# Kernel tuning notes

Measured on AMD Instinct MI355X. Metric: run time of the kernel, lower is better.

Reference implementation:

```python
import jax, jax.numpy as jnp
import numpy as np

B, S, IN, EMB, H = 4, 2048, 256, 512, 8
D = EMB // H
SCALE = 1.0 / np.sqrt(EMB)  # source uses 1/sqrt(embed_size), not head_dim
EPS = 1e-5


def setup_inputs() -> dict:
    key = jax.random.key(0)
    ks = jax.random.split(key, 20)
    def w(k, shape, fan_in):
        return jax.random.normal(k, shape, jnp.float32) * (1.0 / np.sqrt(fan_in))
    inp = {"state_emb": jax.random.normal(ks[0], (B, S, IN), jnp.float32)}
    i = 1
    for p in ("q", "k", "v"):
        inp[f"{p}_W1"] = w(ks[i], (IN, EMB), IN); i += 1
        inp[f"{p}_b1"] = jnp.zeros((EMB,), jnp.float32)
        inp[f"{p}_W2"] = w(ks[i], (EMB, EMB), EMB); i += 1
        inp[f"{p}_b2"] = jnp.zeros((EMB,), jnp.float32)
    inp["f_W1"] = w(ks[i], (EMB, 2 * EMB), EMB); i += 1
    inp["f_b1"] = jnp.zeros((2 * EMB,), jnp.float32)
    inp["f_W2"] = w(ks[i], (2 * EMB, EMB), 2 * EMB); i += 1
    inp["f_b2"] = jnp.zeros((EMB,), jnp.float32)
    inp["ln1_g"] = jnp.ones((EMB,), jnp.float32)
    inp["ln1_b"] = jnp.zeros((EMB,), jnp.float32)
    inp["ln2_g"] = jnp.ones((EMB,), jnp.float32)
    inp["ln2_b"] = jnp.zeros((EMB,), jnp.float32)
    return inp


def _mlp2(x, W1, b1, W2, b2):
    return jax.nn.relu(x @ W1 + b1) @ W2 + b2


def _layernorm(x, g, b):
    mu = jnp.mean(x, axis=-1, keepdims=True)
    var = jnp.mean(jnp.square(x - mu), axis=-1, keepdims=True)
    return (x - mu) * jax.lax.rsqrt(var + EPS) * g + b


def reference(state_emb, q_W1, q_b1, q_W2, q_b2, k_W1, k_b1, k_W2, k_b2,
              v_W1, v_b1, v_W2, v_b2, f_W1, f_b1, f_W2, f_b2,
              ln1_g, ln1_b, ln2_g, ln2_b):
    n, dim = state_emb.shape[0], state_emb.shape[1]
    q = _mlp2(state_emb, q_W1, q_b1, q_W2, q_b2)  # [n, dim, EMB]
    k = _mlp2(state_emb, k_W1, k_b1, k_W2, k_b2)
    v = _mlp2(state_emb, v_W1, v_b1, v_W2, v_b2)
    qh = q.reshape(n, dim, H, D)
    kh = k.reshape(n, dim, H, D)
    vh = v.reshape(n, dim, H, D)
    energy = jnp.einsum('nqhd,nkhd->nhqk', qh, kh)  # [n, H, dim, dim]
    attn = jax.nn.softmax(energy * SCALE, axis=-1)
    ctx = jnp.einsum('nhql,nlhd->nqhd', attn, vh).reshape(n, dim, EMB)
    x = _layernorm(ctx + q, ln1_g, ln1_b)  # residual with queries, per source
    ff = _mlp2(x, f_W1, f_b1, f_W2, f_b2)
    return _layernorm(x + ff, ln2_g, ln2_b)
```

## Files before the change

### kernel.cpp

```cpp
#include <hip/hip_runtime.h>
#include <hip/hip_bf16.h>
#include <math.h>

#define BB   4
#define SS   2048
#define INF_ 256
#define EMB  512
#define NH   8
#define HD   64
#define NT   8192

typedef unsigned short u16;
typedef unsigned int   u32;
typedef __attribute__((ext_vector_type(8))) short bf16x8;
typedef __attribute__((ext_vector_type(8))) unsigned short u16x8;
typedef __attribute__((ext_vector_type(4))) float f32x4;

constexpr float C2  = 0.06375871607f;
constexpr float RB  = 0.005624549f;
constexpr float TB  = 1.00390625f;
constexpr float EPS = 1e-5f;

__device__ __forceinline__ u16 f2bf(float v) {
    __hip_bfloat16 h = __float2bfloat16(v);
    return *(u16*)&h;
}
__device__ __forceinline__ float bf2f(u16 u) {
    __hip_bfloat16 h = *(__hip_bfloat16*)&u;
    return __bfloat162float(h);
}
__device__ __forceinline__ u16 ftrunc_bf(float v) {
    return (u16)(__float_as_uint(v * TB) >> 16);
}
__device__ __forceinline__ f32x4 mfma16(bf16x8 a, bf16x8 b, f32x4 c) {
    return __builtin_amdgcn_mfma_f32_16x16x32_bf16(a, b, c, 0, 0, 0);
}
__device__ __forceinline__ void async16(const void* g, void* l) {
    __builtin_amdgcn_global_load_lds(
        (const __attribute__((address_space(1))) void*)g,
        (__attribute__((address_space(3))) void*)l, 16, 0, 0);
}
__device__ __forceinline__ int derive_flag(const u16* x) {
    const int lane = threadIdx.x & 63;
    const unsigned e = (x[lane * 2] >> 7) & 0xFF;
    float pl = (e == 0 || (e >= 110 && e <= 140)) ? 1.0f : 0.0f;
    #pragma unroll
    for (int o = 1; o < 64; o <<= 1) pl += __shfl_xor(pl, o);
    return pl < 32.0f;
}

__global__ __launch_bounds__(256) void prep(
    const u16* __restrict__ xsrc,
    const void* w0, const void* w1, const void* w2, const void* w3,
    const void* w4, const void* w5, const void* w6, const void* w7,
    const void* p0, const void* p1, const void* p2, const void* p3,
    const void* p4, const void* p5, const void* p6, const void* p7,
    const void* p8, const void* p9, const void* p10, const void* p11,
    u16* __restrict__ xbf, u16* __restrict__ wt1, u16* __restrict__ wt2,
    u16* __restrict__ f1t, u16* __restrict__ f2t, float* __restrict__ small)
{
    const int isf = derive_flag(xsrc);
    const int z = blockIdx.z;
    const int tid = threadIdx.x;

    if (z < 8) {
        int K, M; const void* src; u16* dst;
        switch (z) {
            case 0: K=256;  M=512;  src=w0; dst=wt1;             break;
            case 1: K=256;  M=512;  src=w1; dst=wt1+512*256;     break;
            case 2: K=256;  M=512;  src=w2; dst=wt1+2*512*256;   break;
            case 3: K=512;  M=512;  src=w3; dst=wt2;             break;
            case 4: K=512;  M=512;  src=w4; dst=wt2+512*512;     break;
            case 5: K=512;  M=512;  src=w5; dst=wt2+2*512*512;   break;
            case 6: K=512;  M=1024; src=w6; dst=f1t;             break;
            default:K=1024; M=512;  src=w7; dst=f2t;             break;
        }
        const int m0 = blockIdx.x * 32, k0 = blockIdx.y * 32;
        if (m0 >= M || k0 >= K) return;
        __shared__ u16 t[32][33];
        const int tx = tid & 31, ty = tid >> 5;
        #pragma unroll
        for (int i = 0; i < 4; ++i) {
            const int kk = k0 + ty + i * 8;
            t[ty + i * 8][tx] = isf ? ftrunc_bf(((const float*)src)[(size_t)kk * M + m0 + tx])
                                    : ((const u16*)src)[(size_t)kk * M + m0 + tx];
        }
        __syncthreads();
        #pragma unroll
        for (int i = 0; i < 4; ++i) {
            const int mm = m0 + ty + i * 8;
            dst[(size_t)mm * K + k0 + tx] = t[tx][ty + i * 8];
        }
    } else if (z == 8) {
        const int bid = blockIdx.y * 32 + blockIdx.x;
        const int base = bid * 2048 + tid * 8;
        if (isf) {
            #pragma unroll
            for (int j = 0; j < 8; ++j)
                xbf[base + j] = ftrunc_bf(((const float*)xsrc)[base + j]);
        } else {
            *(u16x8*)&xbf[base] = *(const u16x8*)&xsrc[base];
        }
    } else {
        const int bid = blockIdx.y * 32 + blockIdx.x;
        if (bid >= 28) return;
        const int e = bid * 256 + tid;
        int id, i;
        if (e < 3072)      { id = e >> 9;               i = e & 511;          }
        else if (e < 4096) { id = 6;                    i = e - 3072;         }
        else               { id = 7 + ((e - 4096) >> 9); i = (e - 4096) & 511; }
        const void* src;
        switch (id) {
            case 0: src = p0; break;  case 1: src = p1; break;
            case 2: src = p2; break;  case 3: src = p3; break;
            case 4: src = p4; break;  case 5: src = p5; break;
            case 6: src = p6; break;  case 7: src = p7; break;
            case 8: src = p8; break;  case 9: src = p9; break;
            case 10: src = p10; break; default: src = p11; break;
        }
        small[e] = isf ? ((const float*)src)[i] : bf2f(((const u16*)src)[i]);
    }
}

template <int TR, int TC, bool RELU, bool AWHICH, bool VOUT>
__global__ __launch_bounds__(256) void gemm_bt(
    const u16* __restrict__ Aall, const u16* __restrict__ Wtall,
    const float* __restrict__ ball, u16* __restrict__ out,
    u16* __restrict__ vtb, int N, int K, int M)
{
    constexpr int RT = TR / 32, CT = TC / 32;
    constexpr int AR = TR / 32, BR = TC / 32;
    constexpr int SSTAGE = (TR + TC) * 64;
    constexpr int SELEMS = VOUT ? (SSTAGE > TC * 136 ? SSTAGE : TC * 136) : SSTAGE;
    __shared__ __align__(16) u16 smem[SELEMS];
    u16* sA = smem;
    u16* sB = smem + TR * 64;

    const int mtiles = M / TC;
    const int which = blockIdx.x / mtiles;
    const int colb  = blockIdx.x % mtiles;
    const int row0 = blockIdx.y * TR, col0 = colb * TC;
    const u16* A  = Aall + (AWHICH ? (size_t)which * N * K : 0);
    const u16* Wt = Wtall + (size_t)which * M * K;
    const float* bias = ball + (size_t)which * M;

    const int tid = threadIdx.x;
    const int lane = tid & 63, w = tid >> 6;
    const int wrow = (w & 1) * (TR / 2), wcol = (w >> 1) * (TC / 2);
    const int c = lane & 15, quad = lane >> 4;

    const u16* ap[AR]; const u16* bp[BR];
    #pragma unroll
    for (int i = 0; i < AR; ++i) {
        const int raw = i * 256 + tid, r = raw >> 3, ch = (raw & 7) ^ (r & 7);
        ap[i] = A + (size_t)(row0 + r) * K + ch * 8;
    }
    #pragma unroll
    for (int i = 0; i < BR; ++i) {
        const int raw = i * 256 + tid, r = raw >> 3, ch = (raw & 7) ^ (r & 7);
        bp[i] = Wt + (size_t)(col0 + r) * K + ch * 8;
    }

    f32x4 acc[RT][CT] = {};

    for (int k0 = 0; k0 < K; k0 += 64) {
        __syncthreads();
        #pragma unroll
        for (int i = 0; i < AR; ++i) {
            async16(ap[i], (char*)sA + (i * 256 + tid) * 16);
            ap[i] += 64;
        }
        #pragma unroll
        for (int i = 0; i < BR; ++i) {
            async16(bp[i], (char*)sB + (i * 256 + tid) * 16);
            bp[i] += 64;
        }
        __syncthreads();

        #pragma unroll
        for (int kt = 0; kt < 2; ++kt) {
            bf16x8 af[RT], bfr[CT];
            #pragma unroll
            for (int rt = 0; rt < RT; ++rt) {
                const int r = wrow + rt * 16 + c;
                af[rt] = *(const bf16x8*)&sA[(r * 8 + ((kt * 4 + quad) ^ (r & 7))) * 8];
            }
            #pragma unroll
            for (int ct = 0; ct < CT; ++ct) {
                const int r = wcol + ct * 16 + c;
                bfr[ct] = *(const bf16x8*)&sB[(r * 8 + ((kt * 4 + quad) ^ (r & 7))) * 8];
            }
            #pragma unroll
            for (int rt = 0; rt < RT; ++rt)
                #pragma unroll
                for (int ct = 0; ct < CT; ++ct)
                    acc[rt][ct] = mfma16(af[rt], bfr[ct], acc[rt][ct]);
        }
    }

    if (VOUT && which == 2) {
        __syncthreads();
        #pragma unroll
        for (int rt = 0; rt < RT; ++rt) {
            const int rowb = wrow + rt * 16 + quad * 4;
            #pragma unroll
            for (int ct = 0; ct < CT; ++ct) {
                const int col = wcol + ct * 16 + c;
                const float bb = bias[col0 + col];
                ushort4 pk;
                pk.x = ftrunc_bf(acc[rt][ct][0] + bb);
                pk.y = ftrunc_bf(acc[rt][ct][1] + bb);
                pk.z = ftrunc_bf(acc[rt][ct][2] + bb);
                pk.w = ftrunc_bf(acc[rt][ct][3] + bb);
                *(ushort4*)&smem[col * 136 + rowb] = pk;
            }
        }
        __syncthreads();
        const int dl = tid >> 1, half = tid & 1;
        const int hg = (col0 + dl) >> 6, dd = (col0 + dl) & 63;
        const int bb = row0 >> 11, s0 = row0 & 2047;
        u16* dst = vtb + ((size_t)(bb * NH + hg) * HD + dd) * SS + s0 + half * 64;
        #pragma unroll
        for (int j = 0; j < 8; ++j)
            *(u16x8*)&dst[j * 8] = *(const u16x8*)&smem[dl * 136 + half * 64 + j * 8];
        return;
    }

    const size_t outW = (size_t)which * N * M;
    #pragma unroll
    for (int rt = 0; rt < RT; ++rt) {
        #pragma unroll
        for (int i = 0; i < 4; ++i) {
            const int row = row0 + wrow + rt * 16 + quad * 4 + i;
            #pragma unroll
            for (int ct = 0; ct < CT; ++ct) {
                const int col = col0 + wcol + ct * 16 + c;
                float v = acc[rt][ct][i] + bias[col];
                if (RELU) v = fmaxf(v, 0.0f);
                out[outW + (size_t)row * M + col] = ftrunc_bf(v);
            }
        }
    }
}

__global__ __launch_bounds__(256) void attn_mfma(
    const u16* __restrict__ q, const u16* __restrict__ k,
    const u16* __restrict__ vt, u16* __restrict__ ctx)
{
    __shared__ __align__(16) u16 sK[2][64 * 64];
    __shared__ __align__(16) u16 sV[2][64 * 64];
    __shared__ __align__(16) u16 sP[4][16 * 64];

    const int tid = threadIdx.x;
    const int w = tid >> 6, lane = tid & 63;
    const int c = lane & 15, quad = lane >> 4;
    const int id = blockIdx.x;
    const int slot = id >> 3;
    const int bh = ((id & 7) << 2) | (slot >> 5);
    const int qt = slot & 31;
    const int b = bh >> 3, h = bh & 7;
    const int q0 = qt * 64;
    const size_t tokbase = (size_t)b * SS;
    const int hoff = h * HD;

    const int myq = q0 + w * 16 + c;
    bf16x8 qf[2];
    #pragma unroll
    for (int kt = 0; kt < 2; ++kt)
        qf[kt] = *(const bf16x8*)&q[(tokbase + myq) * EMB + hoff + kt * 32 + quad * 8];

    const u16* kp[2]; const u16* vp[2];
    #pragma unroll
    for (int i = 0; i < 2; ++i) {
        const int raw = i * 256 + tid, rr = raw >> 3, ch = (raw & 7) ^ (rr & 7);
        kp[i] = k + (tokbase + rr) * EMB + hoff + ch * 8;
        vp[i] = vt + ((size_t)(b * NH + h) * HD + rr) * SS + ch * 8;
    }
    auto stage = [&](int buf) {
        #pragma unroll
        for (int i = 0; i < 2; ++i) {
            async16(kp[i], (char*)&sK[buf][0] + (i * 256 + tid) * 16);
            kp[i] += 64 * EMB;
        }
        #pragma unroll
        for (int i = 0; i < 2; ++i) {
            async16(vp[i], (char*)&sV[buf][0] + (i * 256 + tid) * 16);
            vp[i] += 64;
        }
    };
    stage(0);

    float l_lane = 0.0f;
    f32x4 accO[4] = {};

    for (int t = 0; t < SS / 64; ++t) {
        __syncthreads();
        const int buf = t & 1;
        if (t + 1 < SS / 64) stage(buf ^ 1);

        f32x4 accS[4] = {};
        #pragma unroll
        for (int mt = 0; mt < 4; ++mt) {
            const int key = mt * 16 + c;
            #pragma unroll
            for (int kt = 0; kt < 2; ++kt) {
                bf16x8 kf = *(const bf16x8*)&sK[buf][(key * 8 + ((kt * 4 + quad) ^ (key & 7))) * 8];
                accS[mt] = mfma16(kf, qf[kt], accS[mt]);
            }
        }

        u32 pw[8];
        float ls = 0.0f;
        #pragma unroll
        for (int mt = 0; mt < 4; ++mt) {
            const float e0 = __builtin_amdgcn_exp2f(fmaf(accS[mt][0], C2, RB));
            const float e1 = __builtin_amdgcn_exp2f(fmaf(accS[mt][1], C2, RB));
            const float e2 = __builtin_amdgcn_exp2f(fmaf(accS[mt][2], C2, RB));
            const float e3 = __builtin_amdgcn_exp2f(fmaf(accS[mt][3], C2, RB));
            ls += (e0 + e1) + (e2 + e3);
            pw[2 * mt]     = __builtin_amdgcn_perm(__float_as_uint(e1), __float_as_uint(e0), 0x07060302u);
            pw[2 * mt + 1] = __builtin_amdgcn_perm(__float_as_uint(e3), __float_as_uint(e2), 0x07060302u);
        }
        l_lane += ls;

        #pragma unroll
        for (int mt = 0; mt < 4; ++mt) {
            const int chunkW = 2 * mt + (quad >> 1);
            const int blk = c * 8 + (chunkW ^ (c & 7));
            uint2 u; u.x = pw[2 * mt]; u.y = pw[2 * mt + 1];
            *(uint2*)((char*)&sP[w][0] + blk * 16 + 8 * (quad & 1)) = u;
        }

        bf16x8 pf[2];
        #pragma unroll
        for (int kt = 0; kt < 2; ++kt)
            pf[kt] = *(const bf16x8*)&sP[w][(c * 8 + ((kt * 4 + quad) ^ (c & 7))) * 8];
        #pragma unroll
        for (int nt = 0; nt < 4; ++nt) {
            const int d = nt * 16 + c;
            #pragma unroll
            for (int kt = 0; kt < 2; ++kt) {
                bf16x8 vf = *(const bf16x8*)&sV[buf][(d * 8 + ((kt * 4 + quad) ^ (d & 7))) * 8];
                accO[nt] = mfma16(vf, pf[kt], accO[nt]);
            }
        }
    }

    float l = l_lane;
    l += __shfl_xor(l, 16);
    l += __shfl_xor(l, 32);
    const float li = (l > 0.0f) ? (1.0f / l) : 0.0f;

    const int tok = q0 + w * 16 + c;
    u16* dst = ctx + (tokbase + tok) * EMB + hoff + quad * 4;
    #pragma unroll
    for (int nt = 0; nt < 4; ++nt) {
        ushort4 pk;
        pk.x = ftrunc_bf(accO[nt][0] * li);
        pk.y = ftrunc_bf(accO[nt][1] * li);
        pk.z = ftrunc_bf(accO[nt][2] * li);
        pk.w = ftrunc_bf(accO[nt][3] * li);
        *(ushort4*)&dst[nt * 16] = pk;
    }
}

__global__ __launch_bounds__(256) void ln_mid(
    const u16* __restrict__ a, const u16* __restrict__ b2,
    const float* __restrict__ g, const float* __restrict__ be,
    u16* __restrict__ outb)
{
    const int wave = threadIdx.x >> 6, lane = threadIdx.x & 63;
    const size_t row = (size_t)blockIdx.x * 4 + wave;
    const u16x8 av = *(const u16x8*)&a[row * EMB + lane * 8];
    const u16x8 bv = *(const u16x8*)&b2[row * EMB + lane * 8];
    float vals[8], sum = 0.0f;
    #pragma unroll
    for (int i = 0; i < 8; ++i) { vals[i] = bf2f(av[i]) + bf2f(bv[i]); sum += vals[i]; }
    #pragma unroll
    for (int o = 1; o < 64; o <<= 1) sum += __shfl_xor(sum, o);
    const float mu = sum * (1.0f / 512.0f);
    float vs = 0.0f;
    #pragma unroll
    for (int i = 0; i < 8; ++i) { const float d = vals[i] - mu; vs += d * d; }
    #pragma unroll
    for (int o = 1; o < 64; o <<= 1) vs += __shfl_xor(vs, o);
    const float rstd = rsqrtf(vs * (1.0f / 512.0f) + EPS);
    u16x8 ov;
    #pragma unroll
    for (int i = 0; i < 8; ++i) {
        const int col = lane * 8 + i;
        ov[i] = f2bf((vals[i] - mu) * rstd * g[col] + be[col]);
    }
    *(u16x8*)&outb[row * EMB + lane * 8] = ov;
}

__global__ __launch_bounds__(256) void ln_final(
    const u16* __restrict__ a, const u16* __restrict__ b2,
    const float* __restrict__ g, const float* __restrict__ be,
    void* __restrict__ dout, const u16* __restrict__ xsrc)
{
    const int isf = derive_flag(xsrc);
    const int wave = threadIdx.x >> 6, lane = threadIdx.x & 63;
    const size_t row = (size_t)blockIdx.x * 4 + wave;
    const u16x8 av = *(const u16x8*)&a[row * EMB + lane * 8];
    const u16x8 bv = *(const u16x8*)&b2[row * EMB + lane * 8];
    float vals[8], sum = 0.0f;
    #pragma unroll
    for (int i = 0; i < 8; ++i) { vals[i] = bf2f(av[i]) + bf2f(bv[i]); sum += vals[i]; }
    #pragma unroll
    for (int o = 1; o < 64; o <<= 1) sum += __shfl_xor(sum, o);
    const float mu = sum * (1.0f / 512.0f);
    float vs = 0.0f;
    #pragma unroll
    for (int i = 0; i < 8; ++i) { const float d = vals[i] - mu; vs += d * d; }
    #pragma unroll
    for (int o = 1; o < 64; o <<= 1) vs += __shfl_xor(vs, o);
    const float rstd = rsqrtf(vs * (1.0f / 512.0f) + EPS);
    if (isf) {
        #pragma unroll
        for (int i = 0; i < 8; ++i) {
            const int col = lane * 8 + i;
            ((float*)dout)[row * EMB + col] = (vals[i] - mu) * rstd * g[col] + be[col];
        }
    } else {
        u16x8 ov;
        #pragma unroll
        for (int i = 0; i < 8; ++i) {
            const int col = lane * 8 + i;
            ov[i] = f2bf((vals[i] - mu) * rstd * g[col] + be[col]);
        }
        *(u16x8*)&((u16*)dout)[row * EMB + lane * 8] = ov;
    }
}

extern "C" void kernel_launch(void* const* d_in, const int* in_sizes, int n_in,
                              void* d_out, int out_size, void* d_ws, size_t ws_size,
                              hipStream_t stream)
{
    char* ws = (char*)d_ws;
    float* small = (float*)(ws + 0);
    u16*   wt1   = (u16*)(ws + 32768);
    u16*   wt2   = (u16*)(ws + 819200);
    u16*   f1t   = (u16*)(ws + 2392064);
    u16*   f2t   = (u16*)(ws + 3440640);
    u16*   xbf   = (u16*)(ws + 4489216);
    u16*   h3    = (u16*)(ws + 8683520);
    u16*   qkv   = (u16*)(ws + 33849344);
    u16*   vtb   = (u16*)(ws + 59015168);
    u16*   ctxb  = (u16*)(ws + 67403776);
    u16*   x1b   = (u16*)(ws + 75792384);
    u16*   ffb   = (u16*)(ws + 84180992);

    const dim3 blk(256);
    const u16* xsrc = (const u16*)d_in[0];

    prep<<<dim3(32, 32, 10), blk, 0, stream>>>(
        xsrc,
        d_in[1], d_in[5], d_in[9], d_in[3], d_in[7], d_in[11], d_in[13], d_in[15],
        d_in[2], d_in[6], d_in[10], d_in[4], d_in[8], d_in[12],
        d_in[14], d_in[16], d_in[17], d_in[18], d_in[19], d_in[20],
        xbf, wt1, wt2, f1t, f2t, small);

    gemm_bt<128, 128, true, false, false><<<dim3(12, 64), blk, 0, stream>>>(
        xbf, wt1, small + 0, h3, nullptr, NT, INF_, EMB);
    gemm_bt<128, 128, false, true, true><<<dim3(12, 64), blk, 0, stream>>>(
        h3, wt2, small + 1536, qkv, vtb, NT, EMB, EMB);

    attn_mfma<<<dim3(1024), blk, 0, stream>>>(
        qkv, qkv + (size_t)NT * EMB, vtb, ctxb);

    ln_mid<<<NT / 4, blk, 0, stream>>>(ctxb, qkv, small + 4608, small + 5120, x1b);

    u16* h2 = h3;
    gemm_bt<128, 128, true, false, false><<<dim3(8, 64), blk, 0, stream>>>(
        x1b, f1t, small + 3072, h2, nullptr, NT, EMB, 1024);
    gemm_bt<128, 64, false, false, false><<<dim3(8, 64), blk, 0, stream>>>(
        h2, f2t, small + 4096, ffb, nullptr, NT, 1024, EMB);

    ln_final<<<NT / 4, blk, 0, stream>>>(x1b, ffb, small + 5632, small + 6144, d_out, xsrc);
}
```

Measured before the change: 259.3 us.

## Use 64x64 GEMM tiles, pre-scale K, and compute softmax row sums with MFMA

Replaces the templated 128x128/128x64 GEMM with a fixed 64x64-tile GEMM and launches more, smaller blocks with the grid swapped so row tiles vary fastest. The K projection output is pre-multiplied by the softmax exponent constant, which removes the per-element fma before exp2 in attention. The bias term RB is dropped. Attention row sums are now built by an extra MFMA against a ones vector instead of scalar adds and cross-lane shuffles. Smaller tiles give more blocks but less data reuse per tile, and dropping the bias changes the exponent offset, which may affect bf16 rounding or overflow.

```diff
diff --git a/kernel.cpp b/kernel.cpp
--- a/kernel.cpp
+++ b/kernel.cpp
@@ -17,7 +17,6 @@
 typedef __attribute__((ext_vector_type(4))) float f32x4;
 
 constexpr float C2  = 0.06375871607f;
-constexpr float RB  = 0.005624549f;
 constexpr float TB  = 1.00390625f;
 constexpr float EPS = 1e-5f;
 
@@ -122,56 +121,44 @@
     }
 }
 
-template <int TR, int TC, bool RELU, bool AWHICH, bool VOUT>
-__global__ __launch_bounds__(256) void gemm_bt(
+template <bool RELU, bool AWHICH, bool VOUT, bool SCALEK>
+__global__ __launch_bounds__(256) void gemm64(
     const u16* __restrict__ Aall, const u16* __restrict__ Wtall,
     const float* __restrict__ ball, u16* __restrict__ out,
     u16* __restrict__ vtb, int N, int K, int M)
 {
-    constexpr int RT = TR / 32, CT = TC / 32;
-    constexpr int AR = TR / 32, BR = TC / 32;
-    constexpr int SSTAGE = (TR + TC) * 64;
-    constexpr int SELEMS = VOUT ? (SSTAGE > TC * 136 ? SSTAGE : TC * 136) : SSTAGE;
-    __shared__ __align__(16) u16 smem[SELEMS];
-    u16* sA = smem;
-    u16* sB = smem + TR * 64;
-
-    const int mtiles = M / TC;
-    const int which = blockIdx.x / mtiles;
-    const int colb  = blockIdx.x % mtiles;
-    const int row0 = blockIdx.y * TR, col0 = colb * TC;
+    __shared__ __align__(16) u16 sA[64 * 64];
+    __shared__ __align__(16) u16 sB[64 * 64];
+
+    const int mtiles = M >> 6;
+    const int which = blockIdx.y / mtiles;
+    const int colb  = blockIdx.y % mtiles;
+    const int row0 = blockIdx.x << 6, col0 = colb << 6;
     const u16* A  = Aall + (AWHICH ? (size_t)which * N * K : 0);
     const u16* Wt = Wtall + (size_t)which * M * K;
     const float* bias = ball + (size_t)which * M;
 
     const int tid = threadIdx.x;
     const int lane = tid & 63, w = tid >> 6;
-    const int wrow = (w & 1) * (TR / 2), wcol = (w >> 1) * (TC / 2);
+    const int wrow = (w & 1) << 5, wcol = (w >> 1) << 5;
     const int c = lane & 15, quad = lane >> 4;
 
-    const u16* ap[AR]; const u16* bp[BR];
-    #pragma unroll
-    for (int i = 0; i < AR; ++i) {
+    const u16* ap[2]; const u16* bp[2];
+    #pragma unroll
+    for (int i = 0; i < 2; ++i) {
         const int raw = i * 256 + tid, r = raw >> 3, ch = (raw & 7) ^ (r & 7);
         ap[i] = A + (size_t)(row0 + r) * K + ch * 8;
-    }
-    #pragma unroll
-    for (int i = 0; i < BR; ++i) {
-        const int raw = i * 256 + tid, r = raw >> 3, ch = (raw & 7) ^ (r & 7);
         bp[i] = Wt + (size_t)(col0 + r) * K + ch * 8;
     }
 
-    f32x4 acc[RT][CT] = {};
+    f32x4 acc[2][2] = {};
 
     for (int k0 = 0; k0 < K; k0 += 64) {
         __syncthreads();
         #pragma unroll
-        for (int i = 0; i < AR; ++i) {
+        for (int i = 0; i < 2; ++i) {
             async16(ap[i], (char*)sA + (i * 256 + tid) * 16);
             ap[i] += 64;
-        }
-        #pragma unroll
-        for (int i = 0; i < BR; ++i) {
             async16(bp[i], (char*)sB + (i * 256 + tid) * 16);
             bp[i] += 64;
         }
@@ -179,21 +166,21 @@
 
         #pragma unroll
         for (int kt = 0; kt < 2; ++kt) {
-            bf16x8 af[RT], bfr[CT];
-            #pragma unroll
-            for (int rt = 0; rt < RT; ++rt) {
+            bf16x8 af[2], bfr[2];
+            #pragma unroll
+            for (int rt = 0; rt < 2; ++rt) {
                 const int r = wrow + rt * 16 + c;
                 af[rt] = *(const bf16x8*)&sA[(r * 8 + ((kt * 4 + quad) ^ (r & 7))) * 8];
             }
             #pragma unroll
-            for (int ct = 0; ct < CT; ++ct) {
+            for (int ct = 0; ct < 2; ++ct) {
                 const int r = wcol + ct * 16 + c;
                 bfr[ct] = *(const bf16x8*)&sB[(r * 8 + ((kt * 4 + quad) ^ (r & 7))) * 8];
             }
             #pragma unroll
-            for (int rt = 0; rt < RT; ++rt)
+            for (int rt = 0; rt < 2; ++rt)
                 #pragma unroll
-                for (int ct = 0; ct < CT; ++ct)
+                for (int ct = 0; ct < 2; ++ct)
                     acc[rt][ct] = mfma16(af[rt], bfr[ct], acc[rt][ct]);
         }
     }
@@ -201,10 +188,10 @@
     if (VOUT && which == 2) {
         __syncthreads();
         #pragma unroll
-        for (int rt = 0; rt < RT; ++rt) {
+        for (int rt = 0; rt < 2; ++rt) {
             const int rowb = wrow + rt * 16 + quad * 4;
             #pragma unroll
-            for (int ct = 0; ct < CT; ++ct) {
+            for (int ct = 0; ct < 2; ++ct) {
                 const int col = wcol + ct * 16 + c;
                 const float bb = bias[col0 + col];
                 ushort4 pk;
@@ -212,30 +199,31 @@
                 pk.y = ftrunc_bf(acc[rt][ct][1] + bb);
                 pk.z = ftrunc_bf(acc[rt][ct][2] + bb);
                 pk.w = ftrunc_bf(acc[rt][ct][3] + bb);
-                *(ushort4*)&smem[col * 136 + rowb] = pk;
-            }
-        }
-        __syncthreads();
-        const int dl = tid >> 1, half = tid & 1;
+                *(ushort4*)&sA[col * 72 + rowb] = pk;
+            }
+        }
+        __syncthreads();
+        const int dl = tid >> 2, part = tid & 3;
         const int hg = (col0 + dl) >> 6, dd = (col0 + dl) & 63;
         const int bb = row0 >> 11, s0 = row0 & 2047;
-        u16* dst = vtb + ((size_t)(bb * NH + hg) * HD + dd) * SS + s0 + half * 64;
-        #pragma unroll
-        for (int j = 0; j < 8; ++j)
-            *(u16x8*)&dst[j * 8] = *(const u16x8*)&smem[dl * 136 + half * 64 + j * 8];
+        u16* dst = vtb + ((size_t)(bb * NH + hg) * HD + dd) * SS + s0 + part * 16;
+        #pragma unroll
+        for (int j = 0; j < 2; ++j)
+            *(u16x8*)&dst[j * 8] = *(const u16x8*)&sA[dl * 72 + part * 16 + j * 8];
         return;
     }
 
+    const float sc = (SCALEK && which == 1) ? C2 : 1.0f;
     const size_t outW = (size_t)which * N * M;
     #pragma unroll
-    for (int rt = 0; rt < RT; ++rt) {
+    for (int rt = 0; rt < 2; ++rt) {
         #pragma unroll
         for (int i = 0; i < 4; ++i) {
             const int row = row0 + wrow + rt * 16 + quad * 4 + i;
             #pragma unroll
-            for (int ct = 0; ct < CT; ++ct) {
+            for (int ct = 0; ct < 2; ++ct) {
                 const int col = col0 + wcol + ct * 16 + c;
-                float v = acc[rt][ct][i] + bias[col];
+                float v = (acc[rt][ct][i] + bias[col]) * sc;
                 if (RELU) v = fmaxf(v, 0.0f);
                 out[outW + (size_t)row * M + col] = ftrunc_bf(v);
             }
@@ -269,6 +257,10 @@
     for (int kt = 0; kt < 2; ++kt)
         qf[kt] = *(const bf16x8*)&q[(tokbase + myq) * EMB + hoff + kt * 32 + quad * 8];
 
+    union { u32 u[4]; bf16x8 v; } ones;
+    #pragma unroll
+    for (int i = 0; i < 4; ++i) ones.u[i] = 0x3F803F80u;
+
     const u16* kp[2]; const u16* vp[2];
     #pragma unroll
     for (int i = 0; i < 2; ++i) {
@@ -290,8 +282,8 @@
     };
     stage(0);
 
-    float l_lane = 0.0f;
     f32x4 accO[4] = {};
+    f32x4 accL = {};
 
     for (int t = 0; t < SS / 64; ++t) {
         __syncthreads();
@@ -310,18 +302,15 @@
         }
 
         u32 pw[8];
-        float ls = 0.0f;
         #pragma unroll
         for (int mt = 0; mt < 4; ++mt) {
-            const float e0 = __builtin_amdgcn_exp2f(fmaf(accS[mt][0], C2, RB));
-            const float e1 = __builtin_amdgcn_exp2f(fmaf(accS[mt][1], C2, RB));
-            const float e2 = __builtin_amdgcn_exp2f(fmaf(accS[mt][2], C2, RB));
-            const float e3 = __builtin_amdgcn_exp2f(fmaf(accS[mt][3], C2, RB));
-            ls += (e0 + e1) + (e2 + e3);
+            const float e0 = __builtin_amdgcn_exp2f(accS[mt][0]);
+            const float e1 = __builtin_amdgcn_exp2f(accS[mt][1]);
+            const float e2 = __builtin_amdgcn_exp2f(accS[mt][2]);
+            const float e3 = __builtin_amdgcn_exp2f(accS[mt][3]);
             pw[2 * mt]     = __builtin_amdgcn_perm(__float_as_uint(e1), __float_as_uint(e0), 0x07060302u);
             pw[2 * mt + 1] = __builtin_amdgcn_perm(__float_as_uint(e3), __float_as_uint(e2), 0x07060302u);
         }
-        l_lane += ls;
 
         #pragma unroll
         for (int mt = 0; mt < 4; ++mt) {
@@ -335,6 +324,8 @@
         #pragma unroll
         for (int kt = 0; kt < 2; ++kt)
             pf[kt] = *(const bf16x8*)&sP[w][(c * 8 + ((kt * 4 + quad) ^ (c & 7))) * 8];
+        accL = mfma16(ones.v, pf[0], accL);
+        accL = mfma16(ones.v, pf[1], accL);
         #pragma unroll
         for (int nt = 0; nt < 4; ++nt) {
             const int d = nt * 16 + c;
@@ -346,9 +337,7 @@
         }
     }
 
-    float l = l_lane;
-    l += __shfl_xor(l, 16);
-    l += __shfl_xor(l, 32);
+    const float l = accL[0];
     const float li = (l > 0.0f) ? (1.0f / l) : 0.0f;
 
     const int tok = q0 + w * 16 + c;
@@ -461,9 +450,9 @@
         d_in[14], d_in[16], d_in[17], d_in[18], d_in[19], d_in[20],
         xbf, wt1, wt2, f1t, f2t, small);
 
-    gemm_bt<128, 128, true, false, false><<<dim3(12, 64), blk, 0, stream>>>(
+    gemm64<true, false, false, false><<<dim3(128, 24), blk, 0, stream>>>(
         xbf, wt1, small + 0, h3, nullptr, NT, INF_, EMB);
-    gemm_bt<128, 128, false, true, true><<<dim3(12, 64), blk, 0, stream>>>(
+    gemm64<false, true, true, true><<<dim3(128, 24), blk, 0, stream>>>(
         h3, wt2, small + 1536, qkv, vtb, NT, EMB, EMB);
 
     attn_mfma<<<dim3(1024), blk, 0, stream>>>(
@@ -472,9 +461,9 @@
     ln_mid<<<NT / 4, blk, 0, stream>>>(ctxb, qkv, small + 4608, small + 5120, x1b);
 
     u16* h2 = h3;
-    gemm_bt<128, 128, true, false, false><<<dim3(8, 64), blk, 0, stream>>>(
+    gemm64<true, false, false, false><<<dim3(128, 16), blk, 0, stream>>>(
         x1b, f1t, small + 3072, h2, nullptr, NT, EMB, 1024);
-    gemm_bt<128, 64, false, false, false><<<dim3(8, 64), blk, 0, stream>>>(
+    gemm64<false, false, false, false><<<dim3(128, 8), blk, 0, stream>>>(
         h2, f2t, small + 4096, ffb, nullptr, NT, 1024, EMB);
 
     ln_final<<<NT / 4, blk, 0, stream>>>(x1b, ffb, small + 5632, small + 6144, d_out, xsrc);
```

Result: faster. 241.5 us (-6.9%).
